# Kernel optimization log

Measured on AMD Instinct MI355X. Metric: run time of the kernel, lower is better.

The kernel has to match this reference:

```python
import jax, jax.numpy as jnp
import numpy as np


def setup_inputs() -> dict:
    key = jax.random.key(0)
    k1, k2, k3 = jax.random.split(key, 3)
    B, C, H, W = 16, 256, 128, 128
    r = 16  # channels // reduction
    x = jax.random.normal(k1, (B, C, H, W), dtype=jnp.float32)
    # 1x1 conv kernels flattened to linear weights (fan-in scaled init)
    w1 = jax.random.normal(k2, (r, C), dtype=jnp.float32) * (1.0 / np.sqrt(C))
    b1 = jnp.zeros((r,), dtype=jnp.float32)
    w2 = jax.random.normal(k3, (C, r), dtype=jnp.float32) * (1.0 / np.sqrt(r))
    b2 = jnp.zeros((C,), dtype=jnp.float32)
    return {"x": x, "w1": w1, "b1": b1, "w2": w2, "b2": b2}


def reference(x, w1, b1, w2, b2):
    b, c, h, w = x.shape
    n = h * w
    x_flat = x.reshape(b, c, n)
    mu = x_flat.mean(axis=2, keepdims=True)
    xc = x_flat - mu  # [b, c, n]
    # v[b,i] = mean_j cov[b,i,j] where cov = xc @ xc^T / (n-1).
    # Algebraic reassociation: mean_j sum_k xc[i,k] xc[j,k] = sum_k xc[i,k] * s[k] / c
    # with s[k] = sum_j xc[j,k]. Avoids the O(C^2 * n) bmm; same math.
    s = xc.sum(axis=1)  # [b, n]
    denom = jnp.float32(max(1, n - 1) * c)
    v = jnp.einsum('bcn,bn->bc', xc, s) / denom  # [b, c]
    # MLP of 1x1 convs on a [b,c,1,1] descriptor == two linear layers
    h1 = jax.nn.relu(v @ w1.T + b1)              # [b, r]
    gate = jax.nn.sigmoid(h1 @ w2.T + b2)        # [b, c]
    return x * gate[:, :, None, None]
```

## Files before the change

### kernel.cpp

```cpp
#include <hip/hip_runtime.h>

#define B_ 16
#define C_ 256
#define N_ 16384
#define R_ 16
#define W_ 128
#define TPB_ 128
#define R16_ 16

typedef float f32x4 __attribute__((ext_vector_type(4)));

__device__ __forceinline__ float4 ldf4(const float* p) {
    return *reinterpret_cast<const float4*>(p);
}
__device__ __forceinline__ unsigned f2bf(float f) {
    return (__float_as_uint(f) + 0x8000u) >> 16;
}

__global__ __launch_bounds__(512)
void kA(const float* __restrict__ x,
        float* __restrict__ Ppart,
        float* __restrict__ RSpart) {
    const int tile = blockIdx.x;
    const int b = blockIdx.y;
    const int t = threadIdx.x;
    const int lane = t & 63;
    const int w = t >> 6;

    __shared__ ushort tl[C_][130];
    __shared__ float csp[8][64][2];
    __shared__ float colsum[W_];
    __shared__ float phalf[C_][2];

    const float* xt = x + (size_t)b * C_ * N_ + tile * W_ + (lane << 1);

    float2 cs = make_float2(0.f, 0.f);
    const int c0 = w << 5;
#pragma unroll 8
    for (int k = 0; k < 32; ++k) {
        const int c = c0 + k;
        float2 v = *reinterpret_cast<const float2*>(xt + (size_t)c * N_);
        cs.x += v.x; cs.y += v.y;
        *reinterpret_cast<unsigned*>(&tl[c][lane << 1]) =
            f2bf(v.x) | (f2bf(v.y) << 16);
    }
    csp[w][lane][0] = cs.x;
    csp[w][lane][1] = cs.y;
    __syncthreads();

    if (t < W_) {
        float s = 0.f;
#pragma unroll
        for (int ww = 0; ww < 8; ++ww) s += csp[ww][t >> 1][t & 1];
        colsum[t] = s;
    }
    __syncthreads();

    const int c = t & 255, h = t >> 8;
    const unsigned* row = reinterpret_cast<const unsigned*>(&tl[c][0]) + (h << 5);
    const float* csh = colsum + (h << 6);
    float P = 0.f, RS = 0.f;
#pragma unroll
    for (int k = 0; k < 32; ++k) {
        const unsigned pk = row[k];
        const float vx = __uint_as_float(pk << 16);
        const float vy = __uint_as_float(pk & 0xFFFF0000u);
        P += vx * csh[2 * k] + vy * csh[2 * k + 1];
        RS += vx + vy;
    }
    if (h == 1) { phalf[c][0] = P; phalf[c][1] = RS; }
    __syncthreads();
    if (t < C_) {
        P += phalf[t][0];
        RS += phalf[t][1];
        const size_t base = ((size_t)b * TPB_ + tile) * C_;
        Ppart [base + t] = P;
        RSpart[base + t] = RS;
    }
}

__global__ void kB(const float* __restrict__ Ppart,
                   const float* __restrict__ RSpart,
                   const float* __restrict__ w1, const float* __restrict__ b1,
                   const float* __restrict__ w2, const float* __restrict__ b2,
                   float* __restrict__ gate) {
    const int b = blockIdx.x;
    const int t = threadIdx.x;

    float P = 0.f, RS = 0.f;
#pragma unroll 8
    for (int k = 0; k < TPB_; ++k) {
        P  += Ppart [((size_t)b * TPB_ + k) * C_ + t];
        RS += RSpart[((size_t)b * TPB_ + k) * C_ + t];
    }

    __shared__ float red[4];
    float s = RS;
#pragma unroll
    for (int off = 32; off; off >>= 1) s += __shfl_down(s, off, 64);
    if ((t & 63) == 0) red[t >> 6] = s;
    __syncthreads();
    const float T = red[0] + red[1] + red[2] + red[3];
    const float M = T / (float)N_;
    const float denom = (float)(N_ - 1) * (float)C_;

    __shared__ float vl[C_];
    vl[t] = (P - M * RS) / denom;
    __syncthreads();

    __shared__ float hpart[R16_][16];
    __shared__ float h1[R16_];
    {
        const int i = t >> 4, cc = t & 15;
        float a = 0.f;
#pragma unroll
        for (int k = 0; k < 16; ++k)
            a += vl[(cc << 4) + k] * w1[i * C_ + (cc << 4) + k];
        hpart[i][cc] = a;
    }
    __syncthreads();
    if (t < R16_) {
        float a = b1[t];
#pragma unroll
        for (int k = 0; k < 16; ++k) a += hpart[t][k];
        h1[t] = a > 0.f ? a : 0.f;
    }
    __syncthreads();

    float a = b2[t];
#pragma unroll
    for (int i = 0; i < R16_; ++i) a += h1[i] * w2[t * R16_ + i];
    gate[b * C_ + t] = 1.f / (1.f + __expf(-a));
}

__global__ void kC(const float* __restrict__ x,
                   const float* __restrict__ gate,
                   float* __restrict__ out) {
    const size_t total4 = (size_t)B_ * C_ * N_ / 4;
    for (size_t i = (size_t)blockIdx.x * blockDim.x + threadIdx.x; i < total4;
         i += (size_t)gridDim.x * blockDim.x) {
        const int bc = (int)(i >> 12);
        const float g = gate[bc];
        float4 vx = reinterpret_cast<const float4*>(x)[i];
        f32x4 r;
        r.x = vx.x * g; r.y = vx.y * g; r.z = vx.z * g; r.w = vx.w * g;
        __builtin_nontemporal_store(r, reinterpret_cast<f32x4*>(out) + i);
    }
}

extern "C" void kernel_launch(void* const* d_in, const int* in_sizes, int n_in,
                              void* d_out, int out_size, void* d_ws, size_t ws_size,
                              hipStream_t stream) {
    (void)in_sizes; (void)n_in; (void)out_size; (void)ws_size;
    const float* x  = (const float*)d_in[0];
    const float* w1 = (const float*)d_in[1];
    const float* b1 = (const float*)d_in[2];
    const float* w2 = (const float*)d_in[3];
    const float* b2 = (const float*)d_in[4];
    float* out = (float*)d_out;

    float* ws     = (float*)d_ws;
    float* Ppart  = ws;
    float* RSpart = Ppart + (size_t)B_ * TPB_ * C_;
    float* gate   = RSpart + (size_t)B_ * TPB_ * C_;

    hipLaunchKernelGGL(kA, dim3(TPB_, B_), dim3(512), 0, stream,
                       x, Ppart, RSpart);
    hipLaunchKernelGGL(kB, dim3(B_), dim3(256), 0, stream,
                       Ppart, RSpart, w1, b1, w2, b2, gate);
    hipLaunchKernelGGL(kC, dim3(2048), dim3(256), 0, stream,
                       x, gate, out);
}
```

Before: 143.6 us.

## Traverse kC rows in reverse to reuse cached x tail; vectorize kA colsum reads

kC now walks one (b,c) row per block-iteration and processes rows in reverse order, so the last-written part of x, which kA read most recently, is read first while it may still sit in the large last-level cache. The gate load is hoisted to once per row. kA's dot-product loop now reads colsum as float4 and unpacks four bf16 pairs per step, and the bf16 packing uses the HIP intrinsic. The reversed order trades the previous flat grid-stride pattern for per-row loops with a fixed gridDim, which may change load balance.

```diff
diff --git a/kernel.cpp b/kernel.cpp
--- a/kernel.cpp
+++ b/kernel.cpp
@@ -1,20 +1,20 @@
 #include <hip/hip_runtime.h>
+#include <hip/hip_bf16.h>
 
 #define B_ 16
 #define C_ 256
 #define N_ 16384
-#define R_ 16
 #define W_ 128
 #define TPB_ 128
 #define R16_ 16
 
 typedef float f32x4 __attribute__((ext_vector_type(4)));
 
-__device__ __forceinline__ float4 ldf4(const float* p) {
-    return *reinterpret_cast<const float4*>(p);
+__device__ __forceinline__ float bfl(unsigned p) {
+    return __uint_as_float(p << 16);
 }
-__device__ __forceinline__ unsigned f2bf(float f) {
-    return (__float_as_uint(f) + 0x8000u) >> 16;
+__device__ __forceinline__ float bfh(unsigned p) {
+    return __uint_as_float(p & 0xFFFF0000u);
 }
 
 __global__ __launch_bounds__(512)
@@ -41,8 +41,8 @@
         const int c = c0 + k;
         float2 v = *reinterpret_cast<const float2*>(xt + (size_t)c * N_);
         cs.x += v.x; cs.y += v.y;
-        *reinterpret_cast<unsigned*>(&tl[c][lane << 1]) =
-            f2bf(v.x) | (f2bf(v.y) << 16);
+        *reinterpret_cast<__hip_bfloat162*>(&tl[c][lane << 1]) =
+            __float22bfloat162_rn(v);
     }
     csp[w][lane][0] = cs.x;
     csp[w][lane][1] = cs.y;
@@ -58,15 +58,20 @@
 
     const int c = t & 255, h = t >> 8;
     const unsigned* row = reinterpret_cast<const unsigned*>(&tl[c][0]) + (h << 5);
-    const float* csh = colsum + (h << 6);
+    const float4* cs4 = reinterpret_cast<const float4*>(colsum + (h << 6));
     float P = 0.f, RS = 0.f;
 #pragma unroll
-    for (int k = 0; k < 32; ++k) {
-        const unsigned pk = row[k];
-        const float vx = __uint_as_float(pk << 16);
-        const float vy = __uint_as_float(pk & 0xFFFF0000u);
-        P += vx * csh[2 * k] + vy * csh[2 * k + 1];
-        RS += vx + vy;
+    for (int j = 0; j < 8; ++j) {
+        const float4 ca = cs4[2 * j];
+        const float4 cb = cs4[2 * j + 1];
+        const unsigned p0 = row[4 * j + 0];
+        const unsigned p1 = row[4 * j + 1];
+        const unsigned p2 = row[4 * j + 2];
+        const unsigned p3 = row[4 * j + 3];
+        P += bfl(p0) * ca.x + bfh(p0) * ca.y + bfl(p1) * ca.z + bfh(p1) * ca.w
+           + bfl(p2) * cb.x + bfh(p2) * cb.y + bfl(p3) * cb.z + bfh(p3) * cb.w;
+        RS += bfl(p0) + bfh(p0) + bfl(p1) + bfh(p1)
+            + bfl(p2) + bfh(p2) + bfl(p3) + bfh(p3);
     }
     if (h == 1) { phalf[c][0] = P; phalf[c][1] = RS; }
     __syncthreads();
@@ -136,15 +141,18 @@
 __global__ void kC(const float* __restrict__ x,
                    const float* __restrict__ gate,
                    float* __restrict__ out) {
-    const size_t total4 = (size_t)B_ * C_ * N_ / 4;
-    for (size_t i = (size_t)blockIdx.x * blockDim.x + threadIdx.x; i < total4;
-         i += (size_t)gridDim.x * blockDim.x) {
-        const int bc = (int)(i >> 12);
-        const float g = gate[bc];
-        float4 vx = reinterpret_cast<const float4*>(x)[i];
-        f32x4 r;
-        r.x = vx.x * g; r.y = vx.y * g; r.z = vx.z * g; r.w = vx.w * g;
-        __builtin_nontemporal_store(r, reinterpret_cast<f32x4*>(out) + i);
+    const int nrows = B_ * C_;
+    for (int row = blockIdx.x; row < nrows; row += gridDim.x) {
+        const int rr = nrows - 1 - row;
+        const float g = gate[rr];
+        const float4* src = reinterpret_cast<const float4*>(x) + (size_t)rr * 4096;
+        f32x4* dst = reinterpret_cast<f32x4*>(out) + (size_t)rr * 4096;
+        for (int i = threadIdx.x; i < 4096; i += blockDim.x) {
+            float4 vx = src[i];
+            f32x4 r;
+            r.x = vx.x * g; r.y = vx.y * g; r.z = vx.z * g; r.w = vx.w * g;
+            __builtin_nontemporal_store(r, dst + i);
+        }
     }
 }
 
```

New measurement: 140.1 us. 2.4% less time.
